# Kernel tuning notes

Measured on AMD Instinct MI355X. Metric: run time of the kernel, lower is better.

## Reference

```python
import jax, jax.numpy as jnp
import numpy as np

HEADS = 30
HEAD_DIM = 64
DIM = HEADS * HEAD_DIM  # 1920
TXT = 226
VID = 2048
EPS = 1e-5


def setup_inputs() -> dict:
    key = jax.random.key(0)
    ks = jax.random.split(key, 12)
    s = 1.0 / np.sqrt(DIM)
    return {
        "hidden_states": jax.random.normal(ks[0], (1, VID, DIM), jnp.float32),
        "encoder_hidden_states": jax.random.normal(ks[1], (1, TXT, DIM), jnp.float32),
        "rope_cos": jax.random.uniform(ks[2], (VID, HEAD_DIM), jnp.float32, -1.0, 1.0),
        "rope_sin": jax.random.uniform(ks[3], (VID, HEAD_DIM), jnp.float32, -1.0, 1.0),
        "Wq": jax.random.normal(ks[4], (DIM, DIM), jnp.float32) * s,
        "bq": jnp.zeros((DIM,), jnp.float32),
        "Wk": jax.random.normal(ks[5], (DIM, DIM), jnp.float32) * s,
        "bk": jnp.zeros((DIM,), jnp.float32),
        "Wv": jax.random.normal(ks[6], (DIM, DIM), jnp.float32) * s,
        "bv": jnp.zeros((DIM,), jnp.float32),
        "ln_q_w": jnp.ones((HEAD_DIM,), jnp.float32),
        "ln_q_b": jnp.zeros((HEAD_DIM,), jnp.float32),
        "ln_k_w": jnp.ones((HEAD_DIM,), jnp.float32),
        "ln_k_b": jnp.zeros((HEAD_DIM,), jnp.float32),
        "Wo": jax.random.normal(ks[7], (DIM, DIM), jnp.float32) * s,
        "bo": jnp.zeros((DIM,), jnp.float32),
    }


def _layernorm(x, w, b):
    mu = jnp.mean(x, axis=-1, keepdims=True)
    var = jnp.var(x, axis=-1, keepdims=True)
    return (x - mu) * jax.lax.rsqrt(var + EPS) * w + b


def _apply_rope(x, cos, sin):
    # x: [B,H,S_vid,D]; cos/sin: [S_vid,D]. Interleaved-pair rotation (diffusers use_real, unbind_dim=-1).
    xr = x[..., 0::2]
    xi = x[..., 1::2]
    rot = jnp.stack([-xi, xr], axis=-1).reshape(x.shape)
    return x * cos + rot * sin


def reference(hidden_states, encoder_hidden_states, rope_cos, rope_sin,
              Wq, bq, Wk, bk, Wv, bv, ln_q_w, ln_q_b, ln_k_w, ln_k_b, Wo, bo):
    T = encoder_hidden_states.shape[1]
    h = jnp.concatenate([encoder_hidden_states, hidden_states], axis=1)  # [B,S,D]
    B, S, _ = h.shape

    def proj(W, bias):
        y = h @ W.T + bias
        return y.reshape(B, S, HEADS, HEAD_DIM).transpose(0, 2, 1, 3)  # [B,H,S,d]

    q = proj(Wq, bq)
    k = proj(Wk, bk)
    v = proj(Wv, bv)

    q = _layernorm(q, ln_q_w, ln_q_b)
    k = _layernorm(k, ln_k_w, ln_k_b)

    # rotary embedding applied only to the image/video tokens
    q = jnp.concatenate([q[:, :, :T], _apply_rope(q[:, :, T:], rope_cos, rope_sin)], axis=2)
    k = jnp.concatenate([k[:, :, :T], _apply_rope(k[:, :, T:], rope_cos, rope_sin)], axis=2)

    scale = 1.0 / np.sqrt(HEAD_DIM)
    scores = jnp.einsum("bhqd,bhkd->bhqk", q, k) * scale
    attn = jax.nn.softmax(scores, axis=-1)
    out = jnp.einsum("bhqk,bhkd->bhqd", attn, v)

    out = out.transpose(0, 2, 1, 3).reshape(B, S, DIM)
    out = out @ Wo.T + bo
    return out[:, T:], out[:, :T]
```

## Files before the change

### kernel.cpp

```cpp
#include <hip/hip_runtime.h>
#include <hip/hip_bf16.h>

typedef __hip_bfloat16 bf16;
using f32x4 = __attribute__((ext_vector_type(4))) float;
using f32x16 = __attribute__((ext_vector_type(16))) float;
using s16x8 = __attribute__((ext_vector_type(8))) short;

#define S_TOT 2274
#define S_PAD 2304
#define TTXT 226
#define DIMN 1920
#define NH 30
#define HD 64
#define NQKV 5760
#define QSCALE 0.1803368801f

#define GLOAD_LDS16(g, l)                                                              \
  __builtin_amdgcn_global_load_lds((const __attribute__((address_space(1))) void*)(g), \
                                   (__attribute__((address_space(3))) void*)(l), 16, 0, 0)

__global__ void k_prep_h(const float* __restrict__ hid, const float* __restrict__ enc,
                         bf16* __restrict__ h_bf) {
  long i4 = ((long)blockIdx.x * blockDim.x + threadIdx.x) * 4;
  if (i4 >= (long)S_PAD * DIMN) return;
  int s = (int)(i4 / DIMN);
  float4 v = make_float4(0.f, 0.f, 0.f, 0.f);
  if (s < TTXT)
    v = *reinterpret_cast<const float4*>(enc + i4);
  else if (s < S_TOT)
    v = *reinterpret_cast<const float4*>(hid + i4 - (long)TTXT * DIMN);
  union {
    bf16 b[4];
    short4 s4;
  } o;
  o.b[0] = __float2bfloat16(v.x);
  o.b[1] = __float2bfloat16(v.y);
  o.b[2] = __float2bfloat16(v.z);
  o.b[3] = __float2bfloat16(v.w);
  *reinterpret_cast<short4*>(h_bf + i4) = o.s4;
}

__global__ void k_prep_wqkv(const float* __restrict__ Wq, const float* __restrict__ Wk,
                            const float* __restrict__ Wv, bf16* __restrict__ w_bf) {
  long i4 = ((long)blockIdx.x * blockDim.x + threadIdx.x) * 4;
  const long per = (long)DIMN * DIMN;
  if (i4 >= 3 * per) return;
  const float* src = (i4 < per) ? (Wq + i4) : (i4 < 2 * per) ? (Wk + i4 - per) : (Wv + i4 - 2 * per);
  float4 v = *reinterpret_cast<const float4*>(src);
  union {
    bf16 b[4];
    short4 s4;
  } o;
  o.b[0] = __float2bfloat16(v.x);
  o.b[1] = __float2bfloat16(v.y);
  o.b[2] = __float2bfloat16(v.z);
  o.b[3] = __float2bfloat16(v.w);
  *reinterpret_cast<short4*>(w_bf + i4) = o.s4;
}

__global__ void k_prep_wo(const float* __restrict__ Wo, bf16* __restrict__ w_bf) {
  long i4 = ((long)blockIdx.x * blockDim.x + threadIdx.x) * 4;
  if (i4 >= (long)DIMN * DIMN) return;
  float4 v = *reinterpret_cast<const float4*>(Wo + i4);
  union {
    bf16 b[4];
    short4 s4;
  } o;
  o.b[0] = __float2bfloat16(v.x);
  o.b[1] = __float2bfloat16(v.y);
  o.b[2] = __float2bfloat16(v.z);
  o.b[3] = __float2bfloat16(v.w);
  *reinterpret_cast<short4*>(w_bf + i4) = o.s4;
}

#define NKT32 60
#define QBUF 24576
__global__ __launch_bounds__(512, 4) void k_gemm_qkv9(
    const bf16* __restrict__ A, const bf16* __restrict__ B, const float* __restrict__ bq,
    const float* __restrict__ bk, const float* __restrict__ bv, const float* __restrict__ lqw,
    const float* __restrict__ lqb, const float* __restrict__ lkw, const float* __restrict__ lkb,
    const float* __restrict__ cosT, const float* __restrict__ sinT, bf16* __restrict__ qb,
    bf16* __restrict__ kbf, bf16* __restrict__ vt) {
  __shared__ __align__(16) char smem[3 * QBUF];
  const int tid = threadIdx.x;
  const int w = tid >> 6, lane = tid & 63;
  const int clo = lane & 15, lhi = lane >> 4;
  const int wr = w >> 1, wc = w & 1;
  const int m0 = blockIdx.y * 256, n0 = blockIdx.x * 128;

  const int u1 = 512 + tid;
  const long ga0 = (long)(m0 + (tid >> 2)) * DIMN + (((tid & 3) ^ ((tid >> 2) & 3)) * 8);
  const long ga1 = (long)(m0 + (u1 >> 2)) * DIMN + (((u1 & 3) ^ ((u1 >> 2) & 3)) * 8);
  const long gb0 = (long)(n0 + (tid >> 2)) * DIMN + (((tid & 3) ^ ((tid >> 2) & 3)) * 8);
  const int wbase = w * 1024;

  auto stage = [&](int b, int kt) {
    char* Ab = &smem[b * QBUF];
    char* Bb = Ab + 16384;
    const int ko = kt * 32;
    GLOAD_LDS16(A + ga0 + ko, Ab + wbase);
    GLOAD_LDS16(A + ga1 + ko, Ab + 8192 + wbase);
    GLOAD_LDS16(B + gb0 + ko, Bb + wbase);
  };

  auto rdf = [&](const char* base, int row) {
    return *reinterpret_cast<const s16x8*>(base + row * 64 + ((lhi ^ (row & 3)) * 16));
  };

  f32x4 acc[4][4] = {};

  stage(0, 0);
  stage(1, 1);
  for (int t = 0; t < NKT32; ++t) {
    if (t < NKT32 - 1)
      asm volatile("s_waitcnt vmcnt(3)" ::: "memory");
    else
      asm volatile("s_waitcnt vmcnt(0)" ::: "memory");
    __builtin_amdgcn_s_barrier();
    if (t + 2 < NKT32) stage((t + 2) % 3, t + 2);
    const char* Ab = &smem[(t % 3) * QBUF];
    const char* Bb = Ab + 16384;
    s16x8 af[4], bfr[4];
#pragma unroll
    for (int m = 0; m < 4; ++m) af[m] = rdf(Ab, wr * 64 + m * 16 + clo);
#pragma unroll
    for (int n = 0; n < 4; ++n) bfr[n] = rdf(Bb, wc * 64 + n * 16 + clo);
    __builtin_amdgcn_s_setprio(1);
#pragma unroll
    for (int m = 0; m < 4; ++m)
#pragma unroll
      for (int n = 0; n < 4; ++n)
        acc[m][n] = __builtin_amdgcn_mfma_f32_16x16x32_bf16(af[m], bfr[n], acc[m][n], 0, 0, 0);
    __builtin_amdgcn_s_setprio(0);
  }
  __syncthreads();

  const int gcol0 = n0 + wc * 64;
  const int sect = gcol0 / DIMN;
  const int hcol = gcol0 - sect * DIMN;
  const int head = hcol >> 6;
  const int row0 = m0 + wr * 64;

  if (sect < 2) {
    const float* bias = sect ? bk : bq;
    const float* lw = sect ? lkw : lqw;
    const float* lb = sect ? lkb : lqb;
    bf16* dst = sect ? kbf : qb;
    const float oscale = sect ? 1.f : QSCALE;
    float bb[4], lww[4], lbb[4];
#pragma unroll
    for (int n = 0; n < 4; ++n) {
      const int d = (n << 4) + clo;
      bb[n] = bias[hcol + d];
      lww[n] = lw[d];
      lbb[n] = lb[d];
    }
#pragma unroll
    for (int m = 0; m < 4; ++m) {
#pragma unroll
      for (int r = 0; r < 4; ++r) {
        const int row = row0 + m * 16 + lhi * 4 + r;
        float x[4];
#pragma unroll
        for (int n = 0; n < 4; ++n) x[n] = acc[m][n][r] + bb[n];
        float s_ = (x[0] + x[1]) + (x[2] + x[3]);
        float q_ = x[0] * x[0];
        q_ = fmaf(x[1], x[1], q_);
        q_ = fmaf(x[2], x[2], q_);
        q_ = fmaf(x[3], x[3], q_);
#pragma unroll
        for (int off = 1; off <= 8; off <<= 1) {
          s_ += __shfl_xor(s_, off);
          q_ += __shfl_xor(q_, off);
        }
        const float mu = s_ * (1.f / 64.f);
        const float var = q_ * (1.f / 64.f) - mu * mu;
        const float rst = rsqrtf(var + 1e-5f);
        float xn[4];
#pragma unroll
        for (int n = 0; n < 4; ++n) xn[n] = (x[n] - mu) * rst * lww[n] + lbb[n];
        const bool dorope = (row >= TTXT) && (row < S_TOT);
        if (dorope) {
          const float* cr = cosT + (long)(row - TTXT) * HD;
          const float* sr2 = sinT + (long)(row - TTXT) * HD;
#pragma unroll
          for (int n = 0; n < 4; ++n) {
            const int d = (n << 4) + clo;
            const float p = __shfl_xor(xn[n], 1);
            xn[n] = xn[n] * cr[d] + ((clo & 1) ? p : -p) * sr2[d];
          }
        }
#pragma unroll
        for (int n = 0; n < 4; ++n)
          dst[((long)head * S_PAD + row) * HD + (n << 4) + clo] =
              __float2bfloat16(xn[n] * oscale);
      }
    }
  } else {
    float bb[4];
#pragma unroll
    for (int n = 0; n < 4; ++n) bb[n] = bv[hcol + (n << 4) + clo];
    bf16* Lp = reinterpret_cast<bf16*>(smem + w * 9216);
#pragma unroll
    for (int m = 0; m < 4; ++m)
#pragma unroll
      for (int n = 0; n < 4; ++n)
#pragma unroll
        for (int r = 0; r < 4; ++r)
          Lp[((n << 4) + clo) * 72 + m * 16 + lhi * 4 + r] =
              __float2bfloat16(acc[m][n][r] + bb[n]);
    const int dsub = lane >> 3, sc = lane & 7;
#pragma unroll
    for (int it = 0; it < 8; ++it) {
      const int d = it * 8 + dsub;
      s16x8 v = *reinterpret_cast<const s16x8*>(&Lp[d * 72 + sc * 8]);
      *reinterpret_cast<s16x8*>(vt + ((long)head * HD + d) * S_PAD + row0 + sc * 8) = v;
    }
  }
}

#define NKT 30
#define PBUF 32768
__global__ __launch_bounds__(512, 2) void k_gemm_proj8(const bf16* __restrict__ A,
                                                       const bf16* __restrict__ B,
                                                       float* __restrict__ C,
                                                       const float* __restrict__ bias) {
  __shared__ __align__(16) char smem[3 * PBUF];
  const int tid = threadIdx.x;
  const int w = tid >> 6, lane = tid & 63;
  const int clo = lane & 15, lhi = lane >> 4;
  const int wr = w >> 2, wc = w & 3;
  const int m0 = blockIdx.y * 128, n0 = blockIdx.x * 128;

  long ga[2], gb[2];
#pragma unroll
  for (int i = 0; i < 2; ++i) {
    const int s = i * 512 + tid;
    const int row = s >> 3, gch = (s & 7) ^ ((s >> 3) & 7);
    ga[i] = (long)(m0 + row) * DIMN + gch * 8;
    gb[i] = (long)(n0 + row) * DIMN + gch * 8;
  }
  const int wbase = w * 1024;

  auto stage = [&](int b, int kt) {
    char* Ab = &smem[b * PBUF];
    char* Bb = Ab + 16384;
    const int ko = kt * 64;
#pragma unroll
    for (int i = 0; i < 2; ++i) {
      GLOAD_LDS16(A + ga[i] + ko, Ab + i * 8192 + wbase);
      GLOAD_LDS16(B + gb[i] + ko, Bb + i * 8192 + wbase);
    }
  };

  auto rdf = [&](const char* base, int row, int slot) {
    return *reinterpret_cast<const s16x8*>(base + row * 128 + ((slot ^ (row & 7)) * 16));
  };

  f32x4 acc[4][2] = {};

  stage(0, 0);
  stage(1, 1);
  for (int t = 0; t < NKT; ++t) {
    if (t < NKT - 1)
      asm volatile("s_waitcnt vmcnt(4)" ::: "memory");
    else
      asm volatile("s_waitcnt vmcnt(0)" ::: "memory");
    __builtin_amdgcn_s_barrier();
    if (t + 2 < NKT) stage((t + 2) % 3, t + 2);
    const char* Ab = &smem[(t % 3) * PBUF];
    const char* Bb = Ab + 16384;
#pragma unroll
    for (int ks = 0; ks < 2; ++ks) {
      s16x8 af[4], bfr[2];
#pragma unroll
      for (int m = 0; m < 4; ++m) af[m] = rdf(Ab, wr * 64 + m * 16 + clo, ks * 4 + lhi);
#pragma unroll
      for (int n = 0; n < 2; ++n) bfr[n] = rdf(Bb, wc * 32 + n * 16 + clo, ks * 4 + lhi);
      __builtin_amdgcn_s_setprio(1);
#pragma unroll
      for (int m = 0; m < 4; ++m)
#pragma unroll
        for (int n = 0; n < 2; ++n)
          acc[m][n] = __builtin_amdgcn_mfma_f32_16x16x32_bf16(af[m], bfr[n], acc[m][n], 0, 0, 0);
      __builtin_amdgcn_s_setprio(0);
    }
  }
#pragma unroll
  for (int n = 0; n < 2; ++n) {
    const int col = n0 + wc * 32 + n * 16 + clo;
    const float bvv = bias[col];
#pragma unroll
    for (int m = 0; m < 4; ++m) {
#pragma unroll
      for (int r = 0; r < 4; ++r) {
        const int row = m0 + wr * 64 + m * 16 + lhi * 4 + r;
        if (row < S_TOT) {
          const int dst = (row >= TTXT) ? (row - TTXT) : (row + (S_TOT - TTXT));
          C[(long)dst * DIMN + col] = acc[m][n][r] + bvv;
        }
      }
    }
  }
}

__global__ __launch_bounds__(512, 4) void k_flash9(const bf16* __restrict__ qb,
                                                   const bf16* __restrict__ kbf,
                                                   const bf16* __restrict__ vt,
                                                   float* __restrict__ po,
                                                   float* __restrict__ pm,
                                                   float* __restrict__ pl) {
  __shared__ __align__(16) char smem[32768];
  const int h = blockIdx.x, qt = blockIdx.y, ks = blockIdx.z;
  const int tid = threadIdx.x, w = tid >> 6, lane = tid & 63;
  const int l31 = lane & 31, hf = lane >> 5;
  const bf16* Qh = qb + (long)h * S_PAD * HD;
  const bf16* Kh = kbf + (long)h * S_PAD * HD;
  const bf16* Vh = vt + (long)h * HD * S_PAD;
  const int q0w = qt * 256 + w * 32;
  const int T0 = ks * 18;

  s16x8 qf[4];
#pragma unroll
  for (int t = 0; t < 4; ++t)
    qf[t] = *reinterpret_cast<const s16x8*>(Qh + (long)(q0w + l31) * HD + t * 16 + hf * 8);

  f32x16 accO[2] = {};
  f32x16 lacc = {};
  float m_run = -1e30f;

  const s16x8 ones8 = {0x3F80, 0x3F80, 0x3F80, 0x3F80, 0x3F80, 0x3F80, 0x3F80, 0x3F80};

  const int sr = tid >> 3, sc8 = tid & 7;
  const long kg0 = (long)sr * HD + ((sc8 ^ (sr & 7)) * 8);
  const long vg0 = (long)sr * S_PAD + ((sc8 ^ (sr & 7)) * 8);
  const int ldsb = w * 1024;

  auto stage = [&](int b, int kb0) {
    char* Kb = &smem[b * 16384];
    char* Vb = &smem[b * 16384 + 8192];
    GLOAD_LDS16(Kh + (long)kb0 * HD + kg0, Kb + ldsb);
    GLOAD_LDS16(Vh + kb0 + vg0, Vb + ldsb);
  };

  auto ldsrd = [&](const char* base, int row, int c) {
    return *reinterpret_cast<const s16x8*>(base + row * 128 + ((c ^ (row & 7)) * 16));
  };
  auto pk2 = [&](float a, float b) -> unsigned {
    __hip_bfloat162 t = __float22bfloat162_rn(make_float2(a, b));
    return *reinterpret_cast<unsigned*>(&t);
  };

  stage(0, T0 * 64);
  __syncthreads();
  int cur = 0;
  for (int kt = 0; kt < 18; ++kt) {
    const int kb0 = (T0 + kt) * 64;
    if (kt + 1 < 18) stage(cur ^ 1, kb0 + 64);
    const char* Kb = &smem[cur * 16384];
    const char* Vb = &smem[cur * 16384 + 8192];

    f32x16 s0 = {}, s1 = {};
#pragma unroll
    for (int t = 0; t < 4; ++t) {
      s16x8 k0 = ldsrd(Kb, l31, 2 * t + hf);
      s16x8 k1 = ldsrd(Kb, 32 + l31, 2 * t + hf);
      s0 = __builtin_amdgcn_mfma_f32_32x32x16_bf16(k0, qf[t], s0, 0, 0, 0);
      s1 = __builtin_amdgcn_mfma_f32_32x32x16_bf16(k1, qf[t], s1, 0, 0, 0);
    }
    if (kb0 + 64 > S_TOT) {
#pragma unroll
      for (int j = 0; j < 16; ++j) {
        const int key = kb0 + (j & 3) + 8 * (j >> 2) + 4 * hf;
        if (key >= S_TOT) s0[j] = -1e30f;
        if (key + 32 >= S_TOT) s1[j] = -1e30f;
      }
    }
    float a8[8];
#pragma unroll
    for (int i = 0; i < 8; ++i)
      a8[i] = fmaxf(fmaxf(s0[2 * i], s0[2 * i + 1]), fmaxf(s1[2 * i], s1[2 * i + 1]));
    float pmax = fmaxf(fmaxf(fmaxf(a8[0], a8[1]), fmaxf(a8[2], a8[3])),
                       fmaxf(fmaxf(a8[4], a8[5]), fmaxf(a8[6], a8[7])));
    {
      auto r = __builtin_amdgcn_permlane32_swap(__float_as_uint(pmax), __float_as_uint(pmax),
                                                false, false);
      pmax = fmaxf(__uint_as_float(r[0]), __uint_as_float(r[1]));
    }
    if (!__all(pmax - m_run <= 8.f)) {
      const float mnew = fmaxf(m_run, pmax);
      const float corr = exp2f(m_run - mnew);
      m_run = mnew;
#pragma unroll
      for (int j = 0; j < 16; ++j) {
        const float cj = __shfl(corr, (lane & 32) | ((j & 3) + 8 * (j >> 2) + 4 * hf));
        accO[0][j] *= cj;
        accO[1][j] *= cj;
        lacc[j] *= cj;
      }
    }
#pragma unroll
    for (int j = 0; j < 16; ++j) {
      s0[j] = exp2f(s0[j] - m_run);
      s1[j] = exp2f(s1[j] - m_run);
    }
    unsigned gw0[8], gw1[8];
#pragma unroll
    for (int i = 0; i < 4; ++i) {
      gw0[2 * i] = pk2(s0[4 * i], s0[4 * i + 1]);
      gw0[2 * i + 1] = pk2(s0[4 * i + 2], s0[4 * i + 3]);
      gw1[2 * i] = pk2(s1[4 * i], s1[4 * i + 1]);
      gw1[2 * i + 1] = pk2(s1[4 * i + 2], s1[4 * i + 3]);
    }
    s16x8 pa[4];
#pragma unroll
    for (int b = 0; b < 2; ++b) {
      unsigned* gw = b ? gw1 : gw0;
#pragma unroll
      for (int t = 0; t < 2; ++t) {
        auto rA = __builtin_amdgcn_permlane32_swap(gw[4 * t + 0], gw[4 * t + 2], false, false);
        auto rB = __builtin_amdgcn_permlane32_swap(gw[4 * t + 1], gw[4 * t + 3], false, false);
        union {
          unsigned u[4];
          s16x8 v;
        } A;
        A.u[0] = rA[0];
        A.u[1] = rB[0];
        A.u[2] = rA[1];
        A.u[3] = rB[1];
        pa[b * 2 + t] = A.v;
      }
    }
#pragma unroll
    for (int t4 = 0; t4 < 4; ++t4) {
      s16x8 v0 = ldsrd(Vb, l31, 2 * t4 + hf);
      s16x8 v1 = ldsrd(Vb, 32 + l31, 2 * t4 + hf);
      accO[0] = __builtin_amdgcn_mfma_f32_32x32x16_bf16(pa[t4], v0, accO[0], 0, 0, 0);
      accO[1] = __builtin_amdgcn_mfma_f32_32x32x16_bf16(pa[t4], v1, accO[1], 0, 0, 0);
      lacc = __builtin_amdgcn_mfma_f32_32x32x16_bf16(pa[t4], ones8, lacc, 0, 0, 0);
    }
    __syncthreads();
    cur ^= 1;
  }
  const long rowbase = ((long)(ks * NH + h)) * S_PAD + q0w;
  if (hf == 0) pm[rowbase + l31] = m_run;
  if (l31 == 0) {
#pragma unroll
    for (int j = 0; j < 16; ++j) pl[rowbase + (j & 3) + 8 * (j >> 2) + 4 * hf] = lacc[j];
  }
#pragma unroll
  for (int j = 0; j < 16; ++j) {
    const int pat = (j & 3) + 8 * (j >> 2) + 4 * hf;
    float* dst = po + (rowbase + pat) * HD + l31;
    dst[0] = accO[0][j];
    dst[32] = accO[1][j];
  }
}

__global__ __launch_bounds__(256) void k_combine(const float* __restrict__ po,
                                                 const float* __restrict__ pm,
                                                 const float* __restrict__ pl,
                                                 bf16* __restrict__ ao) {
  const int idx = blockIdx.x * 256 + threadIdx.x;
  const int d = idx & 63;
  const int row = (idx >> 6) % S_PAD;
  const int h = idx / (S_PAD * 64);
  if (row >= S_TOT) return;
  const long r1 = (long)h * S_PAD + row;
  const long r2 = (long)(NH + h) * S_PAD + row;
  const float m1 = pm[r1], m2 = pm[r2];
  const float m = fmaxf(m1, m2);
  const float a1 = exp2f(m1 - m), a2 = exp2f(m2 - m);
  const float o = po[r1 * HD + d] * a1 + po[r2 * HD + d] * a2;
  const float l = pl[r1] * a1 + pl[r2] * a2;
  ao[(long)row * DIMN + h * HD + d] = __float2bfloat16(o / l);
}

extern "C" void kernel_launch(void* const* d_in, const int* in_sizes, int n_in, void* d_out,
                              int out_size, void* d_ws, size_t ws_size, hipStream_t stream) {
  const float* hid = (const float*)d_in[0];
  const float* enc = (const float*)d_in[1];
  const float* rc = (const float*)d_in[2];
  const float* rs = (const float*)d_in[3];
  const float* Wq = (const float*)d_in[4];
  const float* bq = (const float*)d_in[5];
  const float* Wk = (const float*)d_in[6];
  const float* bk = (const float*)d_in[7];
  const float* Wv = (const float*)d_in[8];
  const float* bv = (const float*)d_in[9];
  const float* lqw = (const float*)d_in[10];
  const float* lqb = (const float*)d_in[11];
  const float* lkw = (const float*)d_in[12];
  const float* lkb = (const float*)d_in[13];
  const float* Wo = (const float*)d_in[14];
  const float* bo = (const float*)d_in[15];
  float* out = (float*)d_out;

  char* ws = (char*)d_ws;
  size_t off = 0;
  char* scratch = ws + off;
  off += (size_t)S_PAD * NQKV * 4;
  bf16* h_bf = (bf16*)(ws + off);
  off += (size_t)S_PAD * DIMN * 2;
  bf16* wqkv = (bf16*)(ws + off);
  off += (size_t)3 * DIMN * DIMN * 2;
  bf16* wo = (bf16*)(ws + off);
  off += (size_t)DIMN * DIMN * 2;
  bf16* q_bf = (bf16*)(ws + off);
  off += (size_t)NH * S_PAD * HD * 2;
  bf16* k_bf = (bf16*)(ws + off);
  off += (size_t)NH * S_PAD * HD * 2;
  bf16* vt_bf = (bf16*)(ws + off);
  off += (size_t)NH * HD * S_PAD * 2;
  bf16* at_bf = (bf16*)(ws + off);
  off += (size_t)S_PAD * DIMN * 2;

  float* po = (float*)scratch;
  float* pm = (float*)(scratch + (size_t)2 * NH * S_PAD * HD * 4);
  float* pl = pm + (size_t)2 * NH * S_PAD;

  k_prep_h<<<((S_PAD * DIMN) / 4 + 255) / 256, 256, 0, stream>>>(hid, enc, h_bf);
  k_prep_wqkv<<<((3 * DIMN * DIMN) / 4 + 255) / 256, 256, 0, stream>>>(Wq, Wk, Wv, wqkv);
  k_prep_wo<<<((DIMN * DIMN) / 4 + 255) / 256, 256, 0, stream>>>(Wo, wo);
  k_gemm_qkv9<<<dim3(NQKV / 128, S_PAD / 256), 512, 0, stream>>>(
      h_bf, wqkv, bq, bk, bv, lqw, lqb, lkw, lkb, rc, rs, q_bf, k_bf, vt_bf);
  k_flash9<<<dim3(NH, S_PAD / 256, 2), 512, 0, stream>>>(q_bf, k_bf, vt_bf, po, pm, pl);
  k_combine<<<NH * S_PAD * HD / 256, 256, 0, stream>>>(po, pm, pl, at_bf);
  k_gemm_proj8<<<dim3(DIMN / 128, S_PAD / 128), 512, 0, stream>>>(at_bf, wo, out, bo);
}
```

Baseline: 245.9 us.

## Fuse prep kernels, split flash KV three ways, vectorize combine, retile output GEMM

Merges the three fp32-to-bf16 conversion kernels into one launch. Raises the flash-attention KV split from two to three so the grid has more blocks. The combine kernel now merges three partials and reads and writes four elements per thread. The output projection GEMM moves to 256-thread blocks with 128x64 tiles and a K step of 32, roughly doubling block count for better CU fill. Costs include a larger partial-output buffer, extra combine traffic, and aliasing pm/pl onto the h_bf buffer after it is consumed.

```diff
diff --git a/kernel.cpp b/kernel.cpp
--- a/kernel.cpp
+++ b/kernel.cpp
@@ -14,21 +14,44 @@
 #define HD 64
 #define NQKV 5760
 #define QSCALE 0.1803368801f
+#define NSPLIT 3
 
 #define GLOAD_LDS16(g, l)                                                              \
   __builtin_amdgcn_global_load_lds((const __attribute__((address_space(1))) void*)(g), \
                                    (__attribute__((address_space(3))) void*)(l), 16, 0, 0)
 
-__global__ void k_prep_h(const float* __restrict__ hid, const float* __restrict__ enc,
-                         bf16* __restrict__ h_bf) {
+__global__ void k_prep_all(const float* __restrict__ hid, const float* __restrict__ enc,
+                           const float* __restrict__ Wq, const float* __restrict__ Wk,
+                           const float* __restrict__ Wv, const float* __restrict__ Wo,
+                           bf16* __restrict__ h_bf, bf16* __restrict__ wqkv,
+                           bf16* __restrict__ wo_bf) {
+  const long T1 = (long)S_PAD * DIMN;
+  const long PER = (long)DIMN * DIMN;
   long i4 = ((long)blockIdx.x * blockDim.x + threadIdx.x) * 4;
-  if (i4 >= (long)S_PAD * DIMN) return;
-  int s = (int)(i4 / DIMN);
+  if (i4 >= T1 + 4 * PER) return;
   float4 v = make_float4(0.f, 0.f, 0.f, 0.f);
-  if (s < TTXT)
-    v = *reinterpret_cast<const float4*>(enc + i4);
-  else if (s < S_TOT)
-    v = *reinterpret_cast<const float4*>(hid + i4 - (long)TTXT * DIMN);
+  bf16* dst;
+  long di;
+  if (i4 < T1) {
+    int s = (int)(i4 / DIMN);
+    if (s < TTXT)
+      v = *reinterpret_cast<const float4*>(enc + i4);
+    else if (s < S_TOT)
+      v = *reinterpret_cast<const float4*>(hid + i4 - (long)TTXT * DIMN);
+    dst = h_bf;
+    di = i4;
+  } else if (i4 < T1 + 3 * PER) {
+    const long j = i4 - T1;
+    const float* src = (j < PER) ? (Wq + j) : (j < 2 * PER) ? (Wk + j - PER) : (Wv + j - 2 * PER);
+    v = *reinterpret_cast<const float4*>(src);
+    dst = wqkv;
+    di = j;
+  } else {
+    const long j = i4 - T1 - 3 * PER;
+    v = *reinterpret_cast<const float4*>(Wo + j);
+    dst = wo_bf;
+    di = j;
+  }
   union {
     bf16 b[4];
     short4 s4;
@@ -37,40 +60,7 @@
   o.b[1] = __float2bfloat16(v.y);
   o.b[2] = __float2bfloat16(v.z);
   o.b[3] = __float2bfloat16(v.w);
-  *reinterpret_cast<short4*>(h_bf + i4) = o.s4;
-}
-
-__global__ void k_prep_wqkv(const float* __restrict__ Wq, const float* __restrict__ Wk,
-                            const float* __restrict__ Wv, bf16* __restrict__ w_bf) {
-  long i4 = ((long)blockIdx.x * blockDim.x + threadIdx.x) * 4;
-  const long per = (long)DIMN * DIMN;
-  if (i4 >= 3 * per) return;
-  const float* src = (i4 < per) ? (Wq + i4) : (i4 < 2 * per) ? (Wk + i4 - per) : (Wv + i4 - 2 * per);
-  float4 v = *reinterpret_cast<const float4*>(src);
-  union {
-    bf16 b[4];
-    short4 s4;
-  } o;
-  o.b[0] = __float2bfloat16(v.x);
-  o.b[1] = __float2bfloat16(v.y);
-  o.b[2] = __float2bfloat16(v.z);
-  o.b[3] = __float2bfloat16(v.w);
-  *reinterpret_cast<short4*>(w_bf + i4) = o.s4;
-}
-
-__global__ void k_prep_wo(const float* __restrict__ Wo, bf16* __restrict__ w_bf) {
-  long i4 = ((long)blockIdx.x * blockDim.x + threadIdx.x) * 4;
-  if (i4 >= (long)DIMN * DIMN) return;
-  float4 v = *reinterpret_cast<const float4*>(Wo + i4);
-  union {
-    bf16 b[4];
-    short4 s4;
-  } o;
-  o.b[0] = __float2bfloat16(v.x);
-  o.b[1] = __float2bfloat16(v.y);
-  o.b[2] = __float2bfloat16(v.z);
-  o.b[3] = __float2bfloat16(v.w);
-  *reinterpret_cast<short4*>(w_bf + i4) = o.s4;
+  *reinterpret_cast<short4*>(dst + di) = o.s4;
 }
 
 #define NKT32 60
@@ -219,72 +209,61 @@
   }
 }
 
-#define NKT 30
-#define PBUF 32768
-__global__ __launch_bounds__(512, 2) void k_gemm_proj8(const bf16* __restrict__ A,
+__global__ __launch_bounds__(256, 4) void k_gemm_proj9(const bf16* __restrict__ A,
                                                        const bf16* __restrict__ B,
                                                        float* __restrict__ C,
                                                        const float* __restrict__ bias) {
-  __shared__ __align__(16) char smem[3 * PBUF];
+  __shared__ __align__(16) char smem[3 * 12288];
   const int tid = threadIdx.x;
   const int w = tid >> 6, lane = tid & 63;
   const int clo = lane & 15, lhi = lane >> 4;
-  const int wr = w >> 2, wc = w & 3;
-  const int m0 = blockIdx.y * 128, n0 = blockIdx.x * 128;
-
-  long ga[2], gb[2];
-#pragma unroll
-  for (int i = 0; i < 2; ++i) {
-    const int s = i * 512 + tid;
-    const int row = s >> 3, gch = (s & 7) ^ ((s >> 3) & 7);
-    ga[i] = (long)(m0 + row) * DIMN + gch * 8;
-    gb[i] = (long)(n0 + row) * DIMN + gch * 8;
-  }
+  const int wr = w >> 1, wc = w & 1;
+  const int m0 = blockIdx.y * 128, n0 = blockIdx.x * 64;
+
+  const int u1 = 256 + tid;
+  const long ga0 = (long)(m0 + (tid >> 2)) * DIMN + (((tid & 3) ^ ((tid >> 2) & 3)) * 8);
+  const long ga1 = (long)(m0 + (u1 >> 2)) * DIMN + (((u1 & 3) ^ ((u1 >> 2) & 3)) * 8);
+  const long gb0 = (long)(n0 + (tid >> 2)) * DIMN + (((tid & 3) ^ ((tid >> 2) & 3)) * 8);
   const int wbase = w * 1024;
 
   auto stage = [&](int b, int kt) {
-    char* Ab = &smem[b * PBUF];
-    char* Bb = Ab + 16384;
-    const int ko = kt * 64;
-#pragma unroll
-    for (int i = 0; i < 2; ++i) {
-      GLOAD_LDS16(A + ga[i] + ko, Ab + i * 8192 + wbase);
-      GLOAD_LDS16(B + gb[i] + ko, Bb + i * 8192 + wbase);
-    }
-  };
-
-  auto rdf = [&](const char* base, int row, int slot) {
-    return *reinterpret_cast<const s16x8*>(base + row * 128 + ((slot ^ (row & 7)) * 16));
+    char* Ab = &smem[b * 12288];
+    char* Bb = Ab + 8192;
+    const int ko = kt * 32;
+    GLOAD_LDS16(A + ga0 + ko, Ab + wbase);
+    GLOAD_LDS16(A + ga1 + ko, Ab + 4096 + wbase);
+    GLOAD_LDS16(B + gb0 + ko, Bb + wbase);
+  };
+
+  auto rdf = [&](const char* base, int row) {
+    return *reinterpret_cast<const s16x8*>(base + row * 64 + ((lhi ^ (row & 3)) * 16));
   };
 
   f32x4 acc[4][2] = {};
 
   stage(0, 0);
   stage(1, 1);
-  for (int t = 0; t < NKT; ++t) {
-    if (t < NKT - 1)
-      asm volatile("s_waitcnt vmcnt(4)" ::: "memory");
+  for (int t = 0; t < NKT32; ++t) {
+    if (t < NKT32 - 1)
+      asm volatile("s_waitcnt vmcnt(3)" ::: "memory");
     else
       asm volatile("s_waitcnt vmcnt(0)" ::: "memory");
     __builtin_amdgcn_s_barrier();
-    if (t + 2 < NKT) stage((t + 2) % 3, t + 2);
-    const char* Ab = &smem[(t % 3) * PBUF];
-    const char* Bb = Ab + 16384;
-#pragma unroll
-    for (int ks = 0; ks < 2; ++ks) {
-      s16x8 af[4], bfr[2];
-#pragma unroll
-      for (int m = 0; m < 4; ++m) af[m] = rdf(Ab, wr * 64 + m * 16 + clo, ks * 4 + lhi);
-#pragma unroll
-      for (int n = 0; n < 2; ++n) bfr[n] = rdf(Bb, wc * 32 + n * 16 + clo, ks * 4 + lhi);
-      __builtin_amdgcn_s_setprio(1);
-#pragma unroll
-      for (int m = 0; m < 4; ++m)
-#pragma unroll
-        for (int n = 0; n < 2; ++n)
-          acc[m][n] = __builtin_amdgcn_mfma_f32_16x16x32_bf16(af[m], bfr[n], acc[m][n], 0, 0, 0);
-      __builtin_amdgcn_s_setprio(0);
-    }
+    if (t + 2 < NKT32) stage((t + 2) % 3, t + 2);
+    const char* Ab = &smem[(t % 3) * 12288];
+    const char* Bb = Ab + 8192;
+    s16x8 af[4], bfr[2];
+#pragma unroll
+    for (int m = 0; m < 4; ++m) af[m] = rdf(Ab, wr * 64 + m * 16 + clo);
+#pragma unroll
+    for (int n = 0; n < 2; ++n) bfr[n] = rdf(Bb, wc * 32 + n * 16 + clo);
+    __builtin_amdgcn_s_setprio(1);
+#pragma unroll
+    for (int m = 0; m < 4; ++m)
+#pragma unroll
+      for (int n = 0; n < 2; ++n)
+        acc[m][n] = __builtin_amdgcn_mfma_f32_16x16x32_bf16(af[m], bfr[n], acc[m][n], 0, 0, 0);
+    __builtin_amdgcn_s_setprio(0);
   }
 #pragma unroll
   for (int n = 0; n < 2; ++n) {
@@ -304,12 +283,12 @@
   }
 }
 
-__global__ __launch_bounds__(512, 4) void k_flash9(const bf16* __restrict__ qb,
-                                                   const bf16* __restrict__ kbf,
-                                                   const bf16* __restrict__ vt,
-                                                   float* __restrict__ po,
-                                                   float* __restrict__ pm,
-                                                   float* __restrict__ pl) {
+__global__ __launch_bounds__(512, 4) void k_flash10(const bf16* __restrict__ qb,
+                                                    const bf16* __restrict__ kbf,
+                                                    const bf16* __restrict__ vt,
+                                                    float* __restrict__ po,
+                                                    float* __restrict__ pm,
+                                                    float* __restrict__ pl) {
   __shared__ __align__(16) char smem[32768];
   const int h = blockIdx.x, qt = blockIdx.y, ks = blockIdx.z;
   const int tid = threadIdx.x, w = tid >> 6, lane = tid & 63;
@@ -318,7 +297,7 @@
   const bf16* Kh = kbf + (long)h * S_PAD * HD;
   const bf16* Vh = vt + (long)h * HD * S_PAD;
   const int q0w = qt * 256 + w * 32;
-  const int T0 = ks * 18;
+  const int T0 = ks * 12;
 
   s16x8 qf[4];
 #pragma unroll
@@ -354,9 +333,9 @@
   stage(0, T0 * 64);
   __syncthreads();
   int cur = 0;
-  for (int kt = 0; kt < 18; ++kt) {
+  for (int kt = 0; kt < 12; ++kt) {
     const int kb0 = (T0 + kt) * 64;
-    if (kt + 1 < 18) stage(cur ^ 1, kb0 + 64);
+    if (kt + 1 < 12) stage(cur ^ 1, kb0 + 64);
     const char* Kb = &smem[cur * 16384];
     const char* Vb = &smem[cur * 16384 + 8192];
 
@@ -457,23 +436,43 @@
   }
 }
 
-__global__ __launch_bounds__(256) void k_combine(const float* __restrict__ po,
-                                                 const float* __restrict__ pm,
-                                                 const float* __restrict__ pl,
-                                                 bf16* __restrict__ ao) {
+__global__ __launch_bounds__(256) void k_combine3(const float* __restrict__ po,
+                                                  const float* __restrict__ pm,
+                                                  const float* __restrict__ pl,
+                                                  bf16* __restrict__ ao) {
   const int idx = blockIdx.x * 256 + threadIdx.x;
-  const int d = idx & 63;
-  const int row = (idx >> 6) % S_PAD;
-  const int h = idx / (S_PAD * 64);
+  const int d4 = (idx & 15) * 4;
+  const int row = (idx >> 4) % S_PAD;
+  const int h = idx / (S_PAD * 16);
   if (row >= S_TOT) return;
-  const long r1 = (long)h * S_PAD + row;
-  const long r2 = (long)(NH + h) * S_PAD + row;
-  const float m1 = pm[r1], m2 = pm[r2];
-  const float m = fmaxf(m1, m2);
-  const float a1 = exp2f(m1 - m), a2 = exp2f(m2 - m);
-  const float o = po[r1 * HD + d] * a1 + po[r2 * HD + d] * a2;
-  const float l = pl[r1] * a1 + pl[r2] * a2;
-  ao[(long)row * DIMN + h * HD + d] = __float2bfloat16(o / l);
+  long r[NSPLIT];
+#pragma unroll
+  for (int i = 0; i < NSPLIT; ++i) r[i] = ((long)(i * NH + h)) * S_PAD + row;
+  float m = pm[r[0]];
+#pragma unroll
+  for (int i = 1; i < NSPLIT; ++i) m = fmaxf(m, pm[r[i]]);
+  float4 o = make_float4(0.f, 0.f, 0.f, 0.f);
+  float l = 0.f;
+#pragma unroll
+  for (int i = 0; i < NSPLIT; ++i) {
+    const float a = exp2f(pm[r[i]] - m);
+    const float4 p = *reinterpret_cast<const float4*>(po + r[i] * HD + d4);
+    o.x += p.x * a;
+    o.y += p.y * a;
+    o.z += p.z * a;
+    o.w += p.w * a;
+    l += pl[r[i]] * a;
+  }
+  const float inv = 1.f / l;
+  union {
+    bf16 b[4];
+    short4 s4;
+  } ob;
+  ob.b[0] = __float2bfloat16(o.x * inv);
+  ob.b[1] = __float2bfloat16(o.y * inv);
+  ob.b[2] = __float2bfloat16(o.z * inv);
+  ob.b[3] = __float2bfloat16(o.w * inv);
+  *reinterpret_cast<short4*>(ao + (long)row * DIMN + h * HD + d4) = ob.s4;
 }
 
 extern "C" void kernel_launch(void* const* d_in, const int* in_sizes, int n_in, void* d_out,
@@ -498,8 +497,8 @@
 
   char* ws = (char*)d_ws;
   size_t off = 0;
-  char* scratch = ws + off;
-  off += (size_t)S_PAD * NQKV * 4;
+  float* po = (float*)(ws + off);
+  off += (size_t)NSPLIT * NH * S_PAD * HD * 4;
   bf16* h_bf = (bf16*)(ws + off);
   off += (size_t)S_PAD * DIMN * 2;
   bf16* wqkv = (bf16*)(ws + off);
@@ -515,16 +514,15 @@
   bf16* at_bf = (bf16*)(ws + off);
   off += (size_t)S_PAD * DIMN * 2;
 
-  float* po = (float*)scratch;
-  float* pm = (float*)(scratch + (size_t)2 * NH * S_PAD * HD * 4);
-  float* pl = pm + (size_t)2 * NH * S_PAD;
-
-  k_prep_h<<<((S_PAD * DIMN) / 4 + 255) / 256, 256, 0, stream>>>(hid, enc, h_bf);
-  k_prep_wqkv<<<((3 * DIMN * DIMN) / 4 + 255) / 256, 256, 0, stream>>>(Wq, Wk, Wv, wqkv);
-  k_prep_wo<<<((DIMN * DIMN) / 4 + 255) / 256, 256, 0, stream>>>(Wo, wo);
+  float* pm = (float*)h_bf;
+  float* pl = pm + (size_t)NSPLIT * NH * S_PAD;
+
+  const long PREP_N = ((long)S_PAD * DIMN + 4L * DIMN * DIMN) / 4;
+  k_prep_all<<<(int)((PREP_N + 255) / 256), 256, 0, stream>>>(hid, enc, Wq, Wk, Wv, Wo, h_bf,
+                                                              wqkv, wo);
   k_gemm_qkv9<<<dim3(NQKV / 128, S_PAD / 256), 512, 0, stream>>>(
       h_bf, wqkv, bq, bk, bv, lqw, lqb, lkw, lkb, rc, rs, q_bf, k_bf, vt_bf);
-  k_flash9<<<dim3(NH, S_PAD / 256, 2), 512, 0, stream>>>(q_bf, k_bf, vt_bf, po, pm, pl);
-  k_combine<<<NH * S_PAD * HD / 256, 256, 0, stream>>>(po, pm, pl, at_bf);
-  k_gemm_proj8<<<dim3(DIMN / 128, S_PAD / 128), 512, 0, stream>>>(at_bf, wo, out, bo);
+  k_flash10<<<dim3(NH, S_PAD / 256, NSPLIT), 512, 0, stream>>>(q_bf, k_bf, vt_bf, po, pm, pl);
+  k_combine3<<<NH * S_PAD * 16 / 256, 256, 0, stream>>>(po, pm, pl, at_bf);
+  k_gemm_proj9<<<dim3(DIMN / 64, S_PAD / 128), 256, 0, stream>>>(at_bf, wo, out, bo);
 }
```

Result: faster. 234.5 us (-4.7%).
